# Performance work log

Hardware: AMD Instinct MI355X
Metric: run time of the kernel (lower is better)

## Reference

```python
import jax, jax.numpy as jnp
import numpy as np

N_NODES = 100000
N_HIGH = 20000
N_EDGES = 200000
D = 128
HEADS = 4
EPS = 1e-16


def setup_inputs() -> dict:
    key = jax.random.key(0)
    ks = jax.random.split(key, 9)
    s = 1.0 / np.sqrt(D)
    return {
        "n_features": jax.random.normal(ks[0], (N_NODES, D), jnp.float32),
        "W_src": jax.random.normal(ks[1], (D, HEADS * D), jnp.float32) * s,
        "W_dst": jax.random.normal(ks[2], (D, HEADS * D), jnp.float32) * s,
        "att_src": jax.random.normal(ks[3], (1, HEADS, D), jnp.float32) * s,
        "att_dst": jax.random.normal(ks[4], (1, HEADS, D), jnp.float32) * s,
        "W_high": jax.random.normal(ks[5], (D, D), jnp.float32) * s,
        "b_high": jnp.zeros((D,), jnp.float32),
        "src_idx": jax.random.randint(ks[6], (N_EDGES,), 0, N_NODES),
        "dst_idx": jax.random.randint(ks[7], (N_EDGES,), 0, N_HIGH),
    }


def reference(n_features, W_src, W_dst, att_src, att_dst, W_high, b_high, src_idx, dst_idx):
    # --- edge-wise gather of node features ---
    nn_features = n_features[src_idx]                      # [E, D]
    # --- scatter-mean to hyperedge features, gather back per edge ---
    seg_sum = jax.ops.segment_sum(nn_features, dst_idx, num_segments=N_HIGH)
    cnt = jax.ops.segment_sum(jnp.ones((src_idx.shape[0],), nn_features.dtype), dst_idx, num_segments=N_HIGH)
    h_mean = seg_sum / jnp.maximum(cnt, 1.0)[:, None]       # [H, D]
    h_high_e = h_mean[dst_idx]                              # [E, D]
    # --- per-edge multi-head projections ---
    E = src_idx.shape[0]
    h_node = (nn_features @ W_src).reshape(E, HEADS, D)     # [E, h, D]
    h_high = (h_high_e @ W_dst).reshape(E, HEADS, D)        # [E, h, D]
    # --- attention scores ---
    alpha_src = (h_high * att_src).sum(-1)                  # [E, h]
    alpha_dst = (h_node * att_dst).sum(-1)                  # [E, h]
    alpha = jax.nn.leaky_relu(alpha_src + alpha_dst, 0.2)
    # --- segment softmax over edges grouped by hyperedge id ---
    amax = jax.ops.segment_max(alpha, dst_idx, num_segments=N_HIGH)
    alpha = jnp.exp(alpha - amax[dst_idx])
    asum = jax.ops.segment_sum(alpha, dst_idx, num_segments=N_HIGH)
    alpha = alpha / (asum[dst_idx] + EPS)                   # [E, h]
    # --- weight, head-mean, scatter-sum aggregate ---
    h_node = (h_node * alpha[..., None]).mean(axis=1)       # [E, D]
    h_features = jax.ops.segment_sum(h_node, dst_idx, num_segments=N_HIGH)
    h_features = h_features @ W_high + b_high               # [H, D]
    return (h_features, alpha)
```

## Files before the change

### kernel.cpp

```cpp
#include <hip/hip_runtime.h>
#include <math.h>

#define N_NODES 100000
#define N_HIGH  20000
#define N_EDGES 200000
#define D       128
#define HEADS   4
#define EPSF    1e-16f

typedef __attribute__((ext_vector_type(8))) short bf16x8;
typedef __attribute__((ext_vector_type(4))) float f32x4;
typedef unsigned short ushort_t;
typedef unsigned int uint_t;

__device__ __forceinline__ ushort_t bf16_rn(float f) {
  uint_t u = __float_as_uint(f);
  u = u + 0x7FFFu + ((u >> 16) & 1u);
  return (ushort_t)(u >> 16);
}
__device__ __forceinline__ uint_t pack_bf2(float x, float y) {
  return (uint_t)bf16_rn(x) | ((uint_t)bf16_rn(y) << 16);
}
__device__ __forceinline__ float readlane_f(float v, int q) {
  return __uint_as_float(__builtin_amdgcn_readlane(__float_as_uint(v), q));
}

constexpr size_t OFF_VSRC = 0;
constexpr size_t OFF_VDST = OFF_VSRC + 512 * 4;
constexpr size_t OFF_P    = OFF_VDST + 512 * 4;
constexpr size_t OFF_APK  = OFF_P    + 65536 * 4;
constexpr size_t OFF_CNT  = OFF_APK  + 800000 * 4;
constexpr size_t OFF_OFFS = OFF_CNT  + 20000 * 4;
constexpr size_t OFF_FILL = OFF_OFFS + 20004 * 4;
constexpr size_t OFF_SORT = OFF_FILL + 20000 * 4;
constexpr size_t OFF_G    = OFF_SORT + 200000 * 8;
constexpr size_t OFF_NFB  = OFF_G    + 20000 * 512 * 2;
constexpr size_t OFF_AHS  = OFF_NFB  + (size_t)100000 * 128 * 2;

__global__ __launch_bounds__(256) void k_vp(
    const float* __restrict__ Wsrc, const float* __restrict__ Wdst,
    const float* __restrict__ att_src, const float* __restrict__ att_dst,
    const float* __restrict__ Whigh,
    float* __restrict__ v_src, float* __restrict__ v_dst,
    int* __restrict__ cnt, ushort_t* __restrict__ Pt) {
  __shared__ float red[128];
  if (blockIdx.x < 256) {
    int gid = blockIdx.x * 256 + threadIdx.x;
    if (gid < N_HIGH) cnt[gid] = 0;

    int W = blockIdx.x * 4 + (threadIdx.x >> 6);
    int lane = threadIdx.x & 63;
    int which = W >> 9;
    int idx = W & 511;
    int k = idx >> 2, h = idx & 3;
    const float* wrow = (which ? Wdst : Wsrc) + k * (HEADS * D) + h * D;
    const float* arow = (which ? att_src : att_dst) + h * D;
    float2 wv = ((const float2*)wrow)[lane];
    float2 av = ((const float2*)arow)[lane];
    float s = wv.x * av.x + wv.y * av.y;
#pragma unroll
    for (int o = 32; o; o >>= 1) s += __shfl_xor(s, o);
    if (lane == 0) {
      if (which) v_src[k * HEADS + h] = s;
      else       v_dst[k * HEADS + h] = s;
    }
  } else {
    int hk = blockIdx.x - 256;
    int h = hk >> 7, col = hk & 127;
    int d = threadIdx.x & 127, half = threadIdx.x >> 7;
    const float* ws = Wsrc + col * (HEADS * D) + h * D + half * 64;
    const float* wh = Whigh + (size_t)(half * 64) * D + d;
    float s = 0.f;
#pragma unroll 8
    for (int m = 0; m < 64; ++m) s += ws[m] * wh[(size_t)m * D];
    if (half) red[d] = s;
    __syncthreads();
    if (!half) {
      int kp = (col >> 1) * 8 + h * 2 + (col & 1);
      Pt[(size_t)d * 512 + kp] = bf16_rn(0.25f * (s + red[d]));
    }
  }
}

#define NP_BLOCKS 1563
#define H_BLOCKS  782
__global__ __launch_bounds__(256) void k_nodehist(
    const float* __restrict__ nf,
    const float* __restrict__ v_src, const float* __restrict__ v_dst,
    float4* __restrict__ a_pack,
    const int* __restrict__ dst, int* __restrict__ cnt,
    ushort_t* __restrict__ nfb) {
  __shared__ float nfT[128 * 65];
  __shared__ float4 vsf4[128];
  __shared__ float4 vdf4[128];
  __shared__ float part[8][4][64];
  int t = threadIdx.x;
  if (blockIdx.x >= NP_BLOCKS) {
    int e = (blockIdx.x - NP_BLOCKS) * 256 + t;
    if (e < N_EDGES) atomicAdd(&cnt[dst[e]], 1);
    return;
  }
  int n0 = blockIdx.x * 64;

  if (t < 128) vsf4[t] = ((const float4*)v_src)[t];
  else vdf4[t - 128] = ((const float4*)v_dst)[t - 128];

  const float4* nf4 = (const float4*)nf;
#pragma unroll
  for (int j = 0; j < 8; ++j) {
    int f4 = j * 256 + t;
    int r = f4 >> 5, c4 = f4 & 31;
    int n = n0 + r;
    if (n > N_NODES - 1) n = N_NODES - 1;
    float4 g = nf4[(size_t)n * 32 + c4];
    nfT[(c4 * 4 + 0) * 65 + r] = g.x;
    nfT[(c4 * 4 + 1) * 65 + r] = g.y;
    nfT[(c4 * 4 + 2) * 65 + r] = g.z;
    nfT[(c4 * 4 + 3) * 65 + r] = g.w;
    ushort4 hb;
    hb.x = bf16_rn(g.x); hb.y = bf16_rn(g.y);
    hb.z = bf16_rn(g.z); hb.w = bf16_rn(g.w);
    ((ushort4*)nfb)[(size_t)n * 32 + c4] = hb;
  }
  __syncthreads();

  int l = t & 63, w = t >> 6;
  float as[4] = {0.f, 0.f, 0.f, 0.f};
  float ad[4] = {0.f, 0.f, 0.f, 0.f};
#pragma unroll 8
  for (int kk = 0; kk < 32; ++kk) {
    int k = w * 32 + kk;
    float x = nfT[k * 65 + l];
    float4 s4 = vsf4[k];
    float4 d4 = vdf4[k];
    as[0] += x * s4.x; as[1] += x * s4.y; as[2] += x * s4.z; as[3] += x * s4.w;
    ad[0] += x * d4.x; ad[1] += x * d4.y; ad[2] += x * d4.z; ad[3] += x * d4.w;
  }
#pragma unroll
  for (int v = 0; v < 4; ++v) {
    part[v][w][l] = as[v];
    part[v + 4][w][l] = ad[v];
  }
  __syncthreads();

  if (t < 64) {
    int ll = t;
    if (n0 + ll < N_NODES) {
      float4 o;
      o.x = part[0][0][ll] + part[0][1][ll] + part[0][2][ll] + part[0][3][ll];
      o.y = part[1][0][ll] + part[1][1][ll] + part[1][2][ll] + part[1][3][ll];
      o.z = part[2][0][ll] + part[2][1][ll] + part[2][2][ll] + part[2][3][ll];
      o.w = part[3][0][ll] + part[3][1][ll] + part[3][2][ll] + part[3][3][ll];
      a_pack[(size_t)(n0 + ll) * 2] = o;
    }
  } else if (t < 128) {
    int ll = t - 64;
    if (n0 + ll < N_NODES) {
      float4 o;
      o.x = part[4][0][ll] + part[4][1][ll] + part[4][2][ll] + part[4][3][ll];
      o.y = part[5][0][ll] + part[5][1][ll] + part[5][2][ll] + part[5][3][ll];
      o.z = part[6][0][ll] + part[6][1][ll] + part[6][2][ll] + part[6][3][ll];
      o.w = part[7][0][ll] + part[7][1][ll] + part[7][2][ll] + part[7][3][ll];
      a_pack[(size_t)(n0 + ll) * 2 + 1] = o;
    }
  }
}

#define SCAN_PER 20
__global__ __launch_bounds__(1024) void k_scan(
    const int* __restrict__ cnt, int* __restrict__ offs) {
  __shared__ int wsum[16];
  int t = threadIdx.x;
  int lane = t & 63, wv = t >> 6;
  int base = t * SCAN_PER;
  int loc[SCAN_PER];
  int s = 0;
#pragma unroll
  for (int i = 0; i < SCAN_PER; ++i) {
    int idx = base + i;
    loc[i] = (idx < N_HIGH) ? cnt[idx] : 0;
    s += loc[i];
  }
  int tot = s;
#pragma unroll
  for (int o = 1; o < 64; o <<= 1) {
    int v = __shfl_up(tot, o);
    if (lane >= o) tot += v;
  }
  if (lane == 63) wsum[wv] = tot;
  __syncthreads();
  int wpre = 0;
  for (int i = 0; i < 16; ++i) wpre += (i < wv) ? wsum[i] : 0;
  int run = wpre + tot - s;
#pragma unroll
  for (int i = 0; i < SCAN_PER; ++i) {
    int idx = base + i;
    if (idx < N_HIGH) {
      offs[idx] = run;
      run += loc[i];
    }
  }
  if (t == 1023) offs[N_HIGH] = wpre + tot;
}

__global__ void k_scatter(const int* __restrict__ dst, const int* __restrict__ src,
                          const int* __restrict__ offs,
                          int* __restrict__ cnt, int2* __restrict__ sorted) {
  int e = blockIdx.x * blockDim.x + threadIdx.x;
  if (e < N_EDGES) {
    int d = dst[e];
    int pos = offs[d] + (atomicSub(&cnt[d], 1) - 1);
    sorted[pos] = make_int2(e, src[e]);
  }
}

__global__ __launch_bounds__(512) void k_ah(
    const float4* __restrict__ a_pack,
    const int* __restrict__ offs, const int2* __restrict__ sorted,
    float4* __restrict__ ahsum) {
  int j = blockIdx.x * 8 + (threadIdx.x >> 6);
  int lane = threadIdx.x & 63;
  int o0 = offs[j], o1 = offs[j + 1];
  float s[4] = {0.f, 0.f, 0.f, 0.f};
  for (int i = o0 + lane; i < o1; i += 64) {
    int2 es = sorted[i];
    float4 a = a_pack[(size_t)es.y * 2];
    s[0] += a.x; s[1] += a.y; s[2] += a.z; s[3] += a.w;
  }
#pragma unroll
  for (int o = 32; o; o >>= 1)
#pragma unroll
    for (int h = 0; h < 4; ++h) s[h] += __shfl_xor(s[h], o);
  if (lane == 0) ahsum[j] = make_float4(s[0], s[1], s[2], s[3]);
}

#define RS 520
__global__ __launch_bounds__(512) void k_mg(
    const ushort_t* __restrict__ nfb,
    const float4* __restrict__ a_pack,
    const float4* __restrict__ ahsum,
    const int* __restrict__ offs, const int2* __restrict__ sorted,
    const ushort_t* __restrict__ Pt, const float* __restrict__ b,
    float* __restrict__ alpha_out, float* __restrict__ out) {
  __shared__ ushort_t Gl[16 * RS];
  int t = threadIdx.x;
  int w = t >> 6, lane = t & 63;
  int j0 = blockIdx.x * 16;
  int rowA = w * 2, rowB = rowA + 1;
  int jA = j0 + rowA;
  int oA0 = offs[jA], oA1 = offs[jA + 1], oB1 = offs[jA + 2];
  int oB0 = oA1;
  int degA = oA1 - oA0, degB = oB1 - oB0;

  float2 accA[4], accB[4];
#pragma unroll
  for (int h = 0; h < 4; ++h) {
    accA[h] = make_float2(0.f, 0.f);
    accB[h] = make_float2(0.f, 0.f);
  }

  if (degA <= 64 && degB <= 64) {
    bool actA = lane < degA, actB = lane < degB;
    int idxA = min(oA0 + (actA ? lane : 0), N_EDGES - 1);
    int idxB = min(oB0 + (actB ? lane : 0), N_EDGES - 1);
    int2 esA = sorted[idxA];
    int2 esB = sorted[idxB];
    int eA = esA.x, srA = esA.y;
    int eB = esB.x, srB = esB.y;
    float4 z4 = make_float4(0.f, 0.f, 0.f, 0.f);
    float4 adA = z4, adB = z4;
    if (actA) adA = a_pack[(size_t)srA * 2 + 1];
    if (actB) adB = a_pack[(size_t)srB * 2 + 1];
    float4 ahA4 = ahsum[jA];
    float4 ahB4 = ahsum[jA + 1];
    float invA = 1.0f / (float)max(degA, 1);
    float invB = 1.0f / (float)max(degB, 1);

    float exA[4], exB[4];
    {
      float pA0 = ahA4.x * invA + adA.x, pA1 = ahA4.y * invA + adA.y;
      float pA2 = ahA4.z * invA + adA.z, pA3 = ahA4.w * invA + adA.w;
      float pB0 = ahB4.x * invB + adB.x, pB1 = ahB4.y * invB + adB.y;
      float pB2 = ahB4.z * invB + adB.z, pB3 = ahB4.w * invB + adB.w;
      pA0 = pA0 >= 0.f ? pA0 : 0.2f * pA0;
      pA1 = pA1 >= 0.f ? pA1 : 0.2f * pA1;
      pA2 = pA2 >= 0.f ? pA2 : 0.2f * pA2;
      pA3 = pA3 >= 0.f ? pA3 : 0.2f * pA3;
      pB0 = pB0 >= 0.f ? pB0 : 0.2f * pB0;
      pB1 = pB1 >= 0.f ? pB1 : 0.2f * pB1;
      pB2 = pB2 >= 0.f ? pB2 : 0.2f * pB2;
      pB3 = pB3 >= 0.f ? pB3 : 0.2f * pB3;
      exA[0] = actA ? expf(pA0) : 0.f;
      exA[1] = actA ? expf(pA1) : 0.f;
      exA[2] = actA ? expf(pA2) : 0.f;
      exA[3] = actA ? expf(pA3) : 0.f;
      exB[0] = actB ? expf(pB0) : 0.f;
      exB[1] = actB ? expf(pB1) : 0.f;
      exB[2] = actB ? expf(pB2) : 0.f;
      exB[3] = actB ? expf(pB3) : 0.f;
    }
    float seA[4] = {exA[0], exA[1], exA[2], exA[3]};
    float seB[4] = {exB[0], exB[1], exB[2], exB[3]};
#pragma unroll
    for (int o = 32; o; o >>= 1)
#pragma unroll
      for (int h = 0; h < 4; ++h) {
        seA[h] += __shfl_xor(seA[h], o);
        seB[h] += __shfl_xor(seB[h], o);
      }
    float alA[4], alB[4];
#pragma unroll
    for (int h = 0; h < 4; ++h) {
      alA[h] = exA[h] / (seA[h] + EPSF);
      alB[h] = exB[h] / (seB[h] + EPSF);
    }
    if (actA)
      ((float4*)alpha_out)[eA] = make_float4(alA[0], alA[1], alA[2], alA[3]);
    if (actB)
      ((float4*)alpha_out)[eB] = make_float4(alB[0], alB[1], alB[2], alB[3]);

    const uint_t* __restrict__ nfbu = (const uint_t*)nfb;
    int dmax8 = (max(degA, degB) + 7) & ~7;
    for (int c0 = 0; c0 < dmax8; c0 += 8) {
      uint_t xa[8], xb[8];
#pragma unroll
      for (int i = 0; i < 8; ++i) {
        int sqA = __builtin_amdgcn_readlane(srA, c0 + i);
        int sqB = __builtin_amdgcn_readlane(srB, c0 + i);
        xa[i] = nfbu[(size_t)sqA * 64 + lane];
        xb[i] = nfbu[(size_t)sqB * 64 + lane];
      }
#pragma unroll
      for (int i = 0; i < 8; ++i) {
        int q = c0 + i;
        float a0 = readlane_f(alA[0], q);
        float a1 = readlane_f(alA[1], q);
        float a2 = readlane_f(alA[2], q);
        float a3 = readlane_f(alA[3], q);
        float b0 = readlane_f(alB[0], q);
        float b1 = readlane_f(alB[1], q);
        float b2 = readlane_f(alB[2], q);
        float b3 = readlane_f(alB[3], q);
        float xAx = __uint_as_float(xa[i] << 16);
        float xAy = __uint_as_float(xa[i] & 0xFFFF0000u);
        float xBx = __uint_as_float(xb[i] << 16);
        float xBy = __uint_as_float(xb[i] & 0xFFFF0000u);
        accA[0].x += a0 * xAx; accA[0].y += a0 * xAy;
        accA[1].x += a1 * xAx; accA[1].y += a1 * xAy;
        accA[2].x += a2 * xAx; accA[2].y += a2 * xAy;
        accA[3].x += a3 * xAx; accA[3].y += a3 * xAy;
        accB[0].x += b0 * xBx; accB[0].y += b0 * xBy;
        accB[1].x += b1 * xBx; accB[1].y += b1 * xBy;
        accB[2].x += b2 * xBx; accB[2].y += b2 * xBy;
        accB[3].x += b3 * xBx; accB[3].y += b3 * xBy;
      }
    }
  } else {
    for (int pick = 0; pick < 2; ++pick) {
      int o0 = pick ? oB0 : oA0;
      int deg = pick ? degB : degA;
      int jj = jA + pick;
      float2* acc = pick ? accB : accA;

      float4 ah4 = ahsum[jj];
      float invdeg = 1.0f / (float)max(deg, 1);
      float ah[4] = {ah4.x * invdeg, ah4.y * invdeg, ah4.z * invdeg, ah4.w * invdeg};

      float se[4] = {0.f, 0.f, 0.f, 0.f};
      for (int i = lane; i < deg; i += 64) {
        int2 es = sorted[o0 + i];
        float4 a = a_pack[(size_t)es.y * 2 + 1];
        float p[4] = {ah[0] + a.x, ah[1] + a.y, ah[2] + a.z, ah[3] + a.w};
#pragma unroll
        for (int h = 0; h < 4; ++h) {
          float pp = p[h] >= 0.f ? p[h] : 0.2f * p[h];
          se[h] += expf(pp);
        }
      }
#pragma unroll
      for (int o = 32; o; o >>= 1)
#pragma unroll
        for (int h = 0; h < 4; ++h) se[h] += __shfl_xor(se[h], o);
      float inv[4];
#pragma unroll
      for (int h = 0; h < 4; ++h) inv[h] = 1.0f / (se[h] + EPSF);

      for (int c0 = 0; c0 < deg; c0 += 64) {
        int i = c0 + lane;
        float al[4] = {0.f, 0.f, 0.f, 0.f};
        int sreg = 0;
        if (i < deg) {
          int2 es = sorted[o0 + i];
          sreg = es.y;
          float4 a = a_pack[(size_t)sreg * 2 + 1];
          float p[4] = {ah[0] + a.x, ah[1] + a.y, ah[2] + a.z, ah[3] + a.w};
#pragma unroll
          for (int h = 0; h < 4; ++h) {
            float pp = p[h] >= 0.f ? p[h] : 0.2f * p[h];
            al[h] = expf(pp) * inv[h];
          }
          ((float4*)alpha_out)[es.x] = make_float4(al[0], al[1], al[2], al[3]);
        }
        int cl = min(64, deg - c0);
#pragma unroll 2
        for (int q = 0; q < cl; ++q) {
          int sq = __builtin_amdgcn_readlane(sreg, q);
          float a0 = readlane_f(al[0], q);
          float a1 = readlane_f(al[1], q);
          float a2 = readlane_f(al[2], q);
          float a3 = readlane_f(al[3], q);
          uint_t xw = ((const uint_t*)nfb)[(size_t)sq * 64 + lane];
          float xx = __uint_as_float(xw << 16);
          float xy = __uint_as_float(xw & 0xFFFF0000u);
          acc[0].x += a0 * xx; acc[0].y += a0 * xy;
          acc[1].x += a1 * xx; acc[1].y += a1 * xy;
          acc[2].x += a2 * xx; acc[2].y += a2 * xy;
          acc[3].x += a3 * xx; acc[3].y += a3 * xy;
        }
      }
    }
  }
  uint4 gwA, gwB;
  gwA.x = pack_bf2(accA[0].x, accA[0].y);
  gwA.y = pack_bf2(accA[1].x, accA[1].y);
  gwA.z = pack_bf2(accA[2].x, accA[2].y);
  gwA.w = pack_bf2(accA[3].x, accA[3].y);
  gwB.x = pack_bf2(accB[0].x, accB[0].y);
  gwB.y = pack_bf2(accB[1].x, accB[1].y);
  gwB.z = pack_bf2(accB[2].x, accB[2].y);
  gwB.w = pack_bf2(accB[3].x, accB[3].y);
  *(uint4*)&Gl[rowA * RS + lane * 8] = gwA;
  *(uint4*)&Gl[rowB * RS + lane * 8] = gwB;
  __syncthreads();

  int lr = lane & 15, lg = lane >> 4;
  f32x4 c0 = (f32x4){0.f, 0.f, 0.f, 0.f};
  const ushort_t* Pa = Pt + (size_t)lr * 512 + lg * 8 + (size_t)w * 16 * 512;
#pragma unroll
  for (int kt = 0; kt < 16; ++kt) {
    bf16x8 a = *(const bf16x8*)&Gl[lr * RS + kt * 32 + lg * 8];
    bf16x8 b0 = *(const bf16x8*)(Pa + kt * 32);
    c0 = __builtin_amdgcn_mfma_f32_16x16x32_bf16(a, b0, c0, 0, 0, 0);
  }
  int col0 = w * 16 + lr;
  float bb0 = b[col0];
#pragma unroll
  for (int r = 0; r < 4; ++r) {
    int row = j0 + lg * 4 + r;
    out[(size_t)row * 128 + col0] = c0[r] + bb0;
  }
}

extern "C" void kernel_launch(void* const* d_in, const int* in_sizes, int n_in,
                              void* d_out, int out_size, void* d_ws, size_t ws_size,
                              hipStream_t stream) {
  const float* nf      = (const float*)d_in[0];
  const float* Wsrc    = (const float*)d_in[1];
  const float* Wdst    = (const float*)d_in[2];
  const float* att_src = (const float*)d_in[3];
  const float* att_dst = (const float*)d_in[4];
  const float* Whigh   = (const float*)d_in[5];
  const float* bhigh   = (const float*)d_in[6];
  const int*   src     = (const int*)d_in[7];
  const int*   dst     = (const int*)d_in[8];

  char* ws = (char*)d_ws;
  float*    v_src  = (float*)(ws + OFF_VSRC);
  float*    v_dst  = (float*)(ws + OFF_VDST);
  ushort_t* Pt     = (ushort_t*)(ws + OFF_P);
  float4*   a_pack = (float4*)(ws + OFF_APK);
  int*      cnt    = (int*)(ws + OFF_CNT);
  int*      offs   = (int*)(ws + OFF_OFFS);
  int2*     sorted = (int2*)(ws + OFF_SORT);
  ushort_t* nfb    = (ushort_t*)(ws + OFF_NFB);
  float4*   ahsum  = (float4*)(ws + OFF_AHS);

  float* out_h     = (float*)d_out;
  float* out_alpha = (float*)d_out + (size_t)N_HIGH * D;

  k_vp<<<768, 256, 0, stream>>>(Wsrc, Wdst, att_src, att_dst, Whigh,
                                v_src, v_dst, cnt, Pt);
  k_nodehist<<<NP_BLOCKS + H_BLOCKS, 256, 0, stream>>>(
      nf, v_src, v_dst, a_pack, dst, cnt, nfb);
  k_scan<<<1, 1024, 0, stream>>>(cnt, offs);
  k_scatter<<<(N_EDGES + 255) / 256, 256, 0, stream>>>(
      dst, src, offs, cnt, sorted);
  k_ah<<<N_HIGH / 8, 512, 0, stream>>>(a_pack, offs, sorted, ahsum);
  k_mg<<<N_HIGH / 16, 512, 0, stream>>>(nfb, a_pack, ahsum, offs, sorted,
                                        Pt, bhigh, out_alpha, out_h);
}
```

Before: 105.1 us.

## Fuse hyperedge alpha-sum into main kernel and prefetch first gather chunk

Removes the separate k_ah kernel and computes the per-hyperedge sum of source attention terms inside k_mg with a wave shuffle reduction, for both the fast path and the high-degree path. It also issues the first 8 node-feature gathers before the softmax math so their latency overlaps the reductions. This saves one kernel launch and the ahsum round trip through global memory, at the cost of extra a_pack loads and registers in k_mg. The first gather chunk is always loaded even for low-degree segments, using clamped indices.

```diff
diff --git a/kernel.cpp b/kernel.cpp
--- a/kernel.cpp
+++ b/kernel.cpp
@@ -35,7 +35,6 @@
 constexpr size_t OFF_SORT = OFF_FILL + 20000 * 4;
 constexpr size_t OFF_G    = OFF_SORT + 200000 * 8;
 constexpr size_t OFF_NFB  = OFF_G    + 20000 * 512 * 2;
-constexpr size_t OFF_AHS  = OFF_NFB  + (size_t)100000 * 128 * 2;
 
 __global__ __launch_bounds__(256) void k_vp(
     const float* __restrict__ Wsrc, const float* __restrict__ Wdst,
@@ -214,31 +213,10 @@
   }
 }
 
-__global__ __launch_bounds__(512) void k_ah(
-    const float4* __restrict__ a_pack,
-    const int* __restrict__ offs, const int2* __restrict__ sorted,
-    float4* __restrict__ ahsum) {
-  int j = blockIdx.x * 8 + (threadIdx.x >> 6);
-  int lane = threadIdx.x & 63;
-  int o0 = offs[j], o1 = offs[j + 1];
-  float s[4] = {0.f, 0.f, 0.f, 0.f};
-  for (int i = o0 + lane; i < o1; i += 64) {
-    int2 es = sorted[i];
-    float4 a = a_pack[(size_t)es.y * 2];
-    s[0] += a.x; s[1] += a.y; s[2] += a.z; s[3] += a.w;
-  }
-#pragma unroll
-  for (int o = 32; o; o >>= 1)
-#pragma unroll
-    for (int h = 0; h < 4; ++h) s[h] += __shfl_xor(s[h], o);
-  if (lane == 0) ahsum[j] = make_float4(s[0], s[1], s[2], s[3]);
-}
-
 #define RS 520
 __global__ __launch_bounds__(512) void k_mg(
     const ushort_t* __restrict__ nfb,
     const float4* __restrict__ a_pack,
-    const float4* __restrict__ ahsum,
     const int* __restrict__ offs, const int2* __restrict__ sorted,
     const ushort_t* __restrict__ Pt, const float* __restrict__ b,
     float* __restrict__ alpha_out, float* __restrict__ out) {
@@ -267,21 +245,38 @@
     int2 esB = sorted[idxB];
     int eA = esA.x, srA = esA.y;
     int eB = esB.x, srB = esB.y;
+
+    const uint_t* __restrict__ nfbu = (const uint_t*)nfb;
+    uint_t xa0[8], xb0[8];
+#pragma unroll
+    for (int i = 0; i < 8; ++i) {
+      int sqA = __builtin_amdgcn_readlane(srA, i);
+      int sqB = __builtin_amdgcn_readlane(srB, i);
+      xa0[i] = nfbu[(size_t)sqA * 64 + lane];
+      xb0[i] = nfbu[(size_t)sqB * 64 + lane];
+    }
     float4 z4 = make_float4(0.f, 0.f, 0.f, 0.f);
-    float4 adA = z4, adB = z4;
-    if (actA) adA = a_pack[(size_t)srA * 2 + 1];
-    if (actB) adB = a_pack[(size_t)srB * 2 + 1];
-    float4 ahA4 = ahsum[jA];
-    float4 ahB4 = ahsum[jA + 1];
+    float4 asA = z4, adA = z4, asB = z4, adB = z4;
+    if (actA) { asA = a_pack[(size_t)srA * 2]; adA = a_pack[(size_t)srA * 2 + 1]; }
+    if (actB) { asB = a_pack[(size_t)srB * 2]; adB = a_pack[(size_t)srB * 2 + 1]; }
+
+    float sA[4] = {asA.x, asA.y, asA.z, asA.w};
+    float sB[4] = {asB.x, asB.y, asB.z, asB.w};
+#pragma unroll
+    for (int o = 32; o; o >>= 1)
+#pragma unroll
+      for (int h = 0; h < 4; ++h) {
+        sA[h] += __shfl_xor(sA[h], o);
+        sB[h] += __shfl_xor(sB[h], o);
+      }
     float invA = 1.0f / (float)max(degA, 1);
     float invB = 1.0f / (float)max(degB, 1);
-
     float exA[4], exB[4];
     {
-      float pA0 = ahA4.x * invA + adA.x, pA1 = ahA4.y * invA + adA.y;
-      float pA2 = ahA4.z * invA + adA.z, pA3 = ahA4.w * invA + adA.w;
-      float pB0 = ahB4.x * invB + adB.x, pB1 = ahB4.y * invB + adB.y;
-      float pB2 = ahB4.z * invB + adB.z, pB3 = ahB4.w * invB + adB.w;
+      float pA0 = sA[0] * invA + adA.x, pA1 = sA[1] * invA + adA.y;
+      float pA2 = sA[2] * invA + adA.z, pA3 = sA[3] * invA + adA.w;
+      float pB0 = sB[0] * invB + adB.x, pB1 = sB[1] * invB + adB.y;
+      float pB2 = sB[2] * invB + adB.z, pB3 = sB[3] * invB + adB.w;
       pA0 = pA0 >= 0.f ? pA0 : 0.2f * pA0;
       pA1 = pA1 >= 0.f ? pA1 : 0.2f * pA1;
       pA2 = pA2 >= 0.f ? pA2 : 0.2f * pA2;
@@ -319,9 +314,31 @@
     if (actB)
       ((float4*)alpha_out)[eB] = make_float4(alB[0], alB[1], alB[2], alB[3]);
 
-    const uint_t* __restrict__ nfbu = (const uint_t*)nfb;
+#pragma unroll
+    for (int i = 0; i < 8; ++i) {
+      float a0 = readlane_f(alA[0], i);
+      float a1 = readlane_f(alA[1], i);
+      float a2 = readlane_f(alA[2], i);
+      float a3 = readlane_f(alA[3], i);
+      float b0 = readlane_f(alB[0], i);
+      float b1 = readlane_f(alB[1], i);
+      float b2 = readlane_f(alB[2], i);
+      float b3 = readlane_f(alB[3], i);
+      float xAx = __uint_as_float(xa0[i] << 16);
+      float xAy = __uint_as_float(xa0[i] & 0xFFFF0000u);
+      float xBx = __uint_as_float(xb0[i] << 16);
+      float xBy = __uint_as_float(xb0[i] & 0xFFFF0000u);
+      accA[0].x += a0 * xAx; accA[0].y += a0 * xAy;
+      accA[1].x += a1 * xAx; accA[1].y += a1 * xAy;
+      accA[2].x += a2 * xAx; accA[2].y += a2 * xAy;
+      accA[3].x += a3 * xAx; accA[3].y += a3 * xAy;
+      accB[0].x += b0 * xBx; accB[0].y += b0 * xBy;
+      accB[1].x += b1 * xBx; accB[1].y += b1 * xBy;
+      accB[2].x += b2 * xBx; accB[2].y += b2 * xBy;
+      accB[3].x += b3 * xBx; accB[3].y += b3 * xBy;
+    }
     int dmax8 = (max(degA, degB) + 7) & ~7;
-    for (int c0 = 0; c0 < dmax8; c0 += 8) {
+    for (int c0 = 8; c0 < dmax8; c0 += 8) {
       uint_t xa[8], xb[8];
 #pragma unroll
       for (int i = 0; i < 8; ++i) {
@@ -359,12 +376,22 @@
     for (int pick = 0; pick < 2; ++pick) {
       int o0 = pick ? oB0 : oA0;
       int deg = pick ? degB : degA;
-      int jj = jA + pick;
       float2* acc = pick ? accB : accA;
 
-      float4 ah4 = ahsum[jj];
+      float s[4] = {0.f, 0.f, 0.f, 0.f};
+      for (int i = lane; i < deg; i += 64) {
+        int2 es = sorted[o0 + i];
+        float4 a = a_pack[(size_t)es.y * 2];
+        s[0] += a.x; s[1] += a.y; s[2] += a.z; s[3] += a.w;
+      }
+#pragma unroll
+      for (int o = 32; o; o >>= 1)
+#pragma unroll
+        for (int h = 0; h < 4; ++h) s[h] += __shfl_xor(s[h], o);
+      float ah[4];
       float invdeg = 1.0f / (float)max(deg, 1);
-      float ah[4] = {ah4.x * invdeg, ah4.y * invdeg, ah4.z * invdeg, ah4.w * invdeg};
+#pragma unroll
+      for (int h = 0; h < 4; ++h) ah[h] = s[h] * invdeg;
 
       float se[4] = {0.f, 0.f, 0.f, 0.f};
       for (int i = lane; i < deg; i += 64) {
@@ -434,20 +461,20 @@
   __syncthreads();
 
   int lr = lane & 15, lg = lane >> 4;
-  f32x4 c0 = (f32x4){0.f, 0.f, 0.f, 0.f};
+  f32x4 c0v = (f32x4){0.f, 0.f, 0.f, 0.f};
   const ushort_t* Pa = Pt + (size_t)lr * 512 + lg * 8 + (size_t)w * 16 * 512;
 #pragma unroll
   for (int kt = 0; kt < 16; ++kt) {
     bf16x8 a = *(const bf16x8*)&Gl[lr * RS + kt * 32 + lg * 8];
     bf16x8 b0 = *(const bf16x8*)(Pa + kt * 32);
-    c0 = __builtin_amdgcn_mfma_f32_16x16x32_bf16(a, b0, c0, 0, 0, 0);
+    c0v = __builtin_amdgcn_mfma_f32_16x16x32_bf16(a, b0, c0v, 0, 0, 0);
   }
   int col0 = w * 16 + lr;
   float bb0 = b[col0];
 #pragma unroll
   for (int r = 0; r < 4; ++r) {
     int row = j0 + lg * 4 + r;
-    out[(size_t)row * 128 + col0] = c0[r] + bb0;
+    out[(size_t)row * 128 + col0] = c0v[r] + bb0;
   }
 }
 
@@ -473,7 +500,6 @@
   int*      offs   = (int*)(ws + OFF_OFFS);
   int2*     sorted = (int2*)(ws + OFF_SORT);
   ushort_t* nfb    = (ushort_t*)(ws + OFF_NFB);
-  float4*   ahsum  = (float4*)(ws + OFF_AHS);
 
   float* out_h     = (float*)d_out;
   float* out_alpha = (float*)d_out + (size_t)N_HIGH * D;
@@ -485,7 +511,6 @@
   k_scan<<<1, 1024, 0, stream>>>(cnt, offs);
   k_scatter<<<(N_EDGES + 255) / 256, 256, 0, stream>>>(
       dst, src, offs, cnt, sorted);
-  k_ah<<<N_HIGH / 8, 512, 0, stream>>>(a_pack, offs, sorted, ahsum);
-  k_mg<<<N_HIGH / 16, 512, 0, stream>>>(nfb, a_pack, ahsum, offs, sorted,
+  k_mg<<<N_HIGH / 16, 512, 0, stream>>>(nfb, a_pack, offs, sorted,
                                         Pt, bhigh, out_alpha, out_h);
 }
```

Result: faster. 100.5 us (median of 2 runs) (-4.3%).
